# Optimization experiments

Measured on AMD Instinct MI355X. Metric: run time of the kernel, lower is better.

## Reference

```python
import jax, jax.numpy as jnp
import numpy as np

N, E, U, EF, STEPS = 5000, 40000, 64, 16, 4


def setup_inputs() -> dict:
    key = jax.random.key(0)
    ks = jax.random.split(key, 7)
    node_features = jax.random.normal(ks[0], (N, U), dtype=jnp.float32)
    edge_features = jax.random.normal(ks[1], (E, EF), dtype=jnp.float32)
    pair_indices = jax.random.randint(ks[2], (E, 2), 0, N, dtype=jnp.int32)
    # EdgeNetwork params: kernel (efc, nfc*nfc), bias (nfc*nfc,)
    edge_kernel = jax.random.normal(ks[3], (EF, U * U), dtype=jnp.float32) * 0.05
    edge_bias = jnp.zeros((U * U,), dtype=jnp.float32)
    # Keras GRUCell (reset_after=True): kernel (in, 3u), recurrent (u, 3u), bias (2, 3u)
    gru_kernel = jax.random.normal(ks[4], (U, 3 * U), dtype=jnp.float32) * 0.05
    gru_recurrent_kernel = jax.random.normal(ks[5], (U, 3 * U), dtype=jnp.float32) * 0.05
    gru_bias = jnp.zeros((2, 3 * U), dtype=jnp.float32)
    return {
        "node_features": node_features,
        "edge_features": edge_features,
        "pair_indices": pair_indices,
        "edge_kernel": edge_kernel,
        "edge_bias": edge_bias,
        "gru_kernel": gru_kernel,
        "gru_recurrent_kernel": gru_recurrent_kernel,
        "gru_bias": gru_bias,
    }


def _gru_cell(x, h, kernel, rkernel, bias):
    # Keras GRUCell math with reset_after=True
    u = h.shape[-1]
    mx = x @ kernel + bias[0]          # [N, 3u]
    mh = h @ rkernel + bias[1]         # [N, 3u]
    xz, xr, xh = mx[:, :u], mx[:, u:2 * u], mx[:, 2 * u:]
    iz, ir, ih = mh[:, :u], mh[:, u:2 * u], mh[:, 2 * u:]
    z = jax.nn.sigmoid(xz + iz)
    r = jax.nn.sigmoid(xr + ir)
    hh = jnp.tanh(xh + r * ih)
    return z * h + (1.0 - z) * hh


def reference(node_features, edge_features, pair_indices, edge_kernel, edge_bias,
              gru_kernel, gru_recurrent_kernel, gru_bias):
    n = node_features.shape[0]
    u = node_features.shape[1]  # units (pad_length = 0 since nfc == units)
    src = pair_indices[:, 0]
    nbr = pair_indices[:, 1]
    # Edge matrices are loop-invariant: [E, u, u]
    edge_mats = (edge_features @ edge_kernel + edge_bias).reshape(-1, u, u)
    h = node_features
    for _ in range(STEPS):
        nb = h[nbr]                                    # gather [E, u]
        msg = jnp.einsum('eij,ej->ei', edge_mats, nb)  # per-edge matvec
        agg = jax.ops.segment_sum(msg, src, num_segments=n)  # scatter-sum [N, u]
        h = _gru_cell(agg, h, gru_kernel, gru_recurrent_kernel, gru_bias)
    return h
```

## Files before the change

kernel.cpp:

```cpp
#include <hip/hip_runtime.h>
#include <math.h>

#define NN 5000
#define NE 40000
#define UU 64
#define FE 16
#define FEP 17
#define KD (FEP*UU)
#define KH2 (KD/2)
#define LDK (KD+8)
#define NSTEPS 4
#define NT 16
#define NB ((NN+NT-1)/NT)
#define SLOT 40
#define CH 8
#define WBN (UU*KD)
#define GTN (192*64)

typedef _Float16 half8 __attribute__((ext_vector_type(8)));
typedef float f32x4 __attribute__((ext_vector_type(4)));

__device__ __forceinline__ float sigm(float x){ return 1.f/(1.f + __expf(-x)); }
__device__ __forceinline__ int rfl(int x){ return __builtin_amdgcn_readfirstlane(x); }

__global__ void build_k(const float* __restrict__ ek, const float* __restrict__ eb,
                        const float* __restrict__ gk, const float* __restrict__ rk,
                        _Float16* __restrict__ wb, _Float16* __restrict__ gkt,
                        _Float16* __restrict__ rkt, int* __restrict__ deg){
  int tid = blockIdx.x*blockDim.x + threadIdx.x;
  if (tid < NN) deg[tid] = 0;
  if (tid < WBN){
    int i = tid / KD, k = tid - i*KD;
    int f = k >> 6, j = k & 63;
    float v = (f < FE) ? ek[f*4096 + i*64 + j] : eb[i*64 + j];
    wb[tid] = (_Float16)v;
  } else if (tid < WBN + GTN){
    int r = tid - WBN; int n = r >> 6, k = r & 63;
    gkt[r] = (_Float16)gk[k*192 + n];
  } else if (tid < WBN + 2*GTN){
    int r = tid - WBN - GTN; int n = r >> 6, k = r & 63;
    rkt[r] = (_Float16)rk[k*192 + n];
  }
}

__global__ void bucket_k(const int* __restrict__ pair, int* __restrict__ deg,
                         int* __restrict__ eidb){
  int e = blockIdx.x*blockDim.x + threadIdx.x;
  if (e < NE){
    int v = pair[2*e];
    int pos = atomicAdd(&deg[v], 1);
    if (pos < SLOT) eidb[v*SLOT + pos] = e;
  }
}

__global__ __launch_bounds__(512) void prep_k(const int* __restrict__ pair,
                       const float* __restrict__ ef,
                       const int* __restrict__ deg,
                       const int* __restrict__ eidb,
                       int* __restrict__ nbrP, float* __restrict__ efP){
  int w = threadIdx.x >> 6, lane = threadIdx.x & 63;
  int v = blockIdx.x * 8 + w;
  if (v >= NN) return;
  int dg = deg[v]; if (dg > SLOT) dg = SLOT;
  if (lane < dg){
    int e = eidb[v*SLOT + lane];
    int rank = 0;
    for (int j=0; j<dg; ++j){ int ej = eidb[v*SLOT + j]; rank += (ej < e); }
    nbrP[v*SLOT + rank] = pair[2*e + 1];
    const float4* er = (const float4*)(ef + (size_t)e*FE);
    float4* ew = (float4*)(efP + ((size_t)v*SLOT + rank)*FE);
    ew[0] = er[0]; ew[1] = er[1]; ew[2] = er[2]; ew[3] = er[3];
  }
}

__global__ __launch_bounds__(512) void step_k(const float* __restrict__ h_in,
        float* __restrict__ h_out,
        const int* __restrict__ deg, const int* __restrict__ nbrP,
        const float* __restrict__ efP,
        const _Float16* __restrict__ wb, const _Float16* __restrict__ gkt,
        const _Float16* __restrict__ rkt, const float* __restrict__ gb){
  __shared__ _Float16 Gs[NT*LDK];
  __shared__ float    aggP[2][16][68];
  __shared__ _Float16 aggT[16*72];
  __shared__ _Float16 hT[16*72];

  int tid = threadIdx.x;
  int w = tid >> 6, lane = tid & 63;
  int r16 = lane & 15, kh = lane >> 4;
  int vb = blockIdx.x * NT;

  for (int i=tid; i<NT*64; i+=512){
    int lv = i >> 6, j = i & 63; int v = vb + lv;
    hT[lv*72 + j] = (_Float16)((v < NN) ? h_in[(size_t)v*64 + j] : 0.f);
  }

  {
    int v0 = vb + w*2, v1 = v0 + 1;
    int d0 = (v0 < NN) ? deg[v0] : 0; if (d0 > SLOT) d0 = SLOT; d0 = rfl(d0);
    int d1 = (v1 < NN) ? deg[v1] : 0; if (d1 > SLOT) d1 = SLOT; d1 = rfl(d1);
    int nbr0 = (lane < d0) ? nbrP[(size_t)v0*SLOT + lane] : 0;
    int nbr1 = (lane < d1) ? nbrP[(size_t)v1*SLOT + lane] : 0;
    const float* e0base = efP + (size_t)v0*SLOT*FE;
    const float* e1base = efP + (size_t)v1*SLOT*FE;
    float gA[FEP], gB[FEP];
    #pragma unroll
    for (int f=0;f<FEP;++f){ gA[f] = 0.f; gB[f] = 0.f; }
    int dmax = (d0 > d1) ? d0 : d1;
    for (int c0=0; c0<dmax; c0+=CH){
      float hA[CH], hB[CH];
      #pragma unroll
      for (int q=0;q<CH;++q){ int i=c0+q;
        int nA = __shfl(nbr0, i); int nB = __shfl(nbr1, i);
        hA[q] = (i<d0) ? h_in[(size_t)nA*64 + lane] : 0.f;
        hB[q] = (i<d1) ? h_in[(size_t)nB*64 + lane] : 0.f; }
      #pragma unroll
      for (int q=0;q<CH;++q){ int i=c0+q;
        if (i<d0){
          const float4* er = (const float4*)(e0base + (size_t)i*FE);
          float4 e0 = er[0], e1 = er[1], e2 = er[2], e3 = er[3];
          float hj = hA[q];
          gA[ 0]=fmaf(e0.x,hj,gA[ 0]); gA[ 1]=fmaf(e0.y,hj,gA[ 1]);
          gA[ 2]=fmaf(e0.z,hj,gA[ 2]); gA[ 3]=fmaf(e0.w,hj,gA[ 3]);
          gA[ 4]=fmaf(e1.x,hj,gA[ 4]); gA[ 5]=fmaf(e1.y,hj,gA[ 5]);
          gA[ 6]=fmaf(e1.z,hj,gA[ 6]); gA[ 7]=fmaf(e1.w,hj,gA[ 7]);
          gA[ 8]=fmaf(e2.x,hj,gA[ 8]); gA[ 9]=fmaf(e2.y,hj,gA[ 9]);
          gA[10]=fmaf(e2.z,hj,gA[10]); gA[11]=fmaf(e2.w,hj,gA[11]);
          gA[12]=fmaf(e3.x,hj,gA[12]); gA[13]=fmaf(e3.y,hj,gA[13]);
          gA[14]=fmaf(e3.z,hj,gA[14]); gA[15]=fmaf(e3.w,hj,gA[15]);
          gA[16] += hj;
        }
        if (i<d1){
          const float4* er = (const float4*)(e1base + (size_t)i*FE);
          float4 e0 = er[0], e1 = er[1], e2 = er[2], e3 = er[3];
          float hj = hB[q];
          gB[ 0]=fmaf(e0.x,hj,gB[ 0]); gB[ 1]=fmaf(e0.y,hj,gB[ 1]);
          gB[ 2]=fmaf(e0.z,hj,gB[ 2]); gB[ 3]=fmaf(e0.w,hj,gB[ 3]);
          gB[ 4]=fmaf(e1.x,hj,gB[ 4]); gB[ 5]=fmaf(e1.y,hj,gB[ 5]);
          gB[ 6]=fmaf(e1.z,hj,gB[ 6]); gB[ 7]=fmaf(e1.w,hj,gB[ 7]);
          gB[ 8]=fmaf(e2.x,hj,gB[ 8]); gB[ 9]=fmaf(e2.y,hj,gB[ 9]);
          gB[10]=fmaf(e2.z,hj,gB[10]); gB[11]=fmaf(e2.w,hj,gB[11]);
          gB[12]=fmaf(e3.x,hj,gB[12]); gB[13]=fmaf(e3.y,hj,gB[13]);
          gB[14]=fmaf(e3.z,hj,gB[14]); gB[15]=fmaf(e3.w,hj,gB[15]);
          gB[16] += hj;
        } }
    }
    #pragma unroll
    for (int f=0;f<FEP;++f){
      Gs[(w*2  )*LDK + f*64 + lane] = (_Float16)gA[f];
      Gs[(w*2+1)*LDK + f*64 + lane] = (_Float16)gB[f];
    }
  }
  __syncthreads();

  {
    int cg = w & 3, khalf = w >> 2;
    int koff = khalf * KH2;
    f32x4 acc = {0.f,0.f,0.f,0.f};
    const _Float16* ap = Gs + r16*LDK + koff + kh*8;
    const _Float16* bp = wb + (size_t)(cg*16 + r16)*KD + koff + kh*8;
    #pragma unroll 4
    for (int k0=0; k0<KH2; k0+=32){
      half8 a = *(const half8*)(ap + k0);
      half8 b = *(const half8*)(bp + k0);
      acc = __builtin_amdgcn_mfma_f32_16x16x32_f16(a, b, acc, 0, 0, 0);
    }
    #pragma unroll
    for (int r=0;r<4;++r) aggP[khalf][kh*4+r][cg*16 + r16] = acc[r];
  }
  __syncthreads();

  for (int i=tid; i<NT*64; i+=512){
    int rw = i >> 6, cl = i & 63;
    aggT[rw*72 + cl] = (_Float16)(aggP[0][rw][cl] + aggP[1][rw][cl]);
  }
  __syncthreads();

  if (w < 4){
    int uw = w*16 + r16;
    const _Float16* az = aggT + r16*72 + kh*8;
    const _Float16* ah = hT   + r16*72 + kh*8;
    f32x4 mxz={0.f,0.f,0.f,0.f}, mxr=mxz, mxh=mxz, mhz=mxz, mhr=mxz, mhh=mxz;
    #pragma unroll
    for (int ks=0; ks<2; ++ks){
      half8 aa = *(const half8*)(az + ks*32);
      half8 hh = *(const half8*)(ah + ks*32);
      half8 bz = *(const half8*)(gkt + (size_t)(      uw)*64 + ks*32 + kh*8);
      half8 br = *(const half8*)(gkt + (size_t)( 64 + uw)*64 + ks*32 + kh*8);
      half8 bh = *(const half8*)(gkt + (size_t)(128 + uw)*64 + ks*32 + kh*8);
      half8 cz = *(const half8*)(rkt + (size_t)(      uw)*64 + ks*32 + kh*8);
      half8 cr = *(const half8*)(rkt + (size_t)( 64 + uw)*64 + ks*32 + kh*8);
      half8 ch = *(const half8*)(rkt + (size_t)(128 + uw)*64 + ks*32 + kh*8);
      mxz = __builtin_amdgcn_mfma_f32_16x16x32_f16(aa, bz, mxz, 0,0,0);
      mxr = __builtin_amdgcn_mfma_f32_16x16x32_f16(aa, br, mxr, 0,0,0);
      mxh = __builtin_amdgcn_mfma_f32_16x16x32_f16(aa, bh, mxh, 0,0,0);
      mhz = __builtin_amdgcn_mfma_f32_16x16x32_f16(hh, cz, mhz, 0,0,0);
      mhr = __builtin_amdgcn_mfma_f32_16x16x32_f16(hh, cr, mhr, 0,0,0);
      mhh = __builtin_amdgcn_mfma_f32_16x16x32_f16(hh, ch, mhh, 0,0,0);
    }
    float b0z = gb[uw],      b0r = gb[64+uw],  b0h = gb[128+uw];
    float b1z = gb[192+uw],  b1r = gb[256+uw], b1h = gb[320+uw];
    #pragma unroll
    for (int r=0;r<4;++r){
      int row = vb + kh*4 + r;
      if (row < NN){
        float z  = sigm(mxz[r] + b0z + mhz[r] + b1z);
        float rr = sigm(mxr[r] + b0r + mhr[r] + b1r);
        float hc = tanhf(mxh[r] + b0h + rr*(mhh[r] + b1h));
        float hold = h_in[(size_t)row*64 + uw];
        h_out[(size_t)row*64 + uw] = z*hold + (1.f - z)*hc;
      }
    }
  }
}

extern "C" void kernel_launch(void* const* d_in, const int* in_sizes, int n_in,
                              void* d_out, int out_size, void* d_ws, size_t ws_size,
                              hipStream_t stream){
  const float* nodef = (const float*)d_in[0];
  const float* edgef = (const float*)d_in[1];
  const int*   pair  = (const int*)  d_in[2];
  const float* ek    = (const float*)d_in[3];
  const float* ebias = (const float*)d_in[4];
  const float* gk    = (const float*)d_in[5];
  const float* rk    = (const float*)d_in[6];
  const float* gb    = (const float*)d_in[7];

  char* ws = (char*)d_ws;
  size_t o = 0;
  auto carve = [&](size_t bytes)->char*{
    char* p = ws + o; o = (o + bytes + 255) & ~255ULL; return p; };
  int*      deg  = (int*)     carve(NN*sizeof(int));
  int*      eidb = (int*)     carve((size_t)NN*SLOT*sizeof(int));
  int*      nbrP = (int*)     carve((size_t)NN*SLOT*sizeof(int));
  float*    efP  = (float*)   carve((size_t)NN*SLOT*FE*sizeof(float));
  _Float16* wb   = (_Float16*)carve((size_t)WBN*sizeof(_Float16));
  _Float16* gkt  = (_Float16*)carve((size_t)GTN*sizeof(_Float16));
  _Float16* rkt  = (_Float16*)carve((size_t)GTN*sizeof(_Float16));
  float*    hA   = (float*)   carve((size_t)NN*UU*sizeof(float));
  float*    hB   = (float*)   carve((size_t)NN*UU*sizeof(float));

  build_k <<<(WBN+2*GTN+255)/256, 256, 0, stream>>>(ek, ebias, gk, rk, wb, gkt, rkt, deg);
  bucket_k<<<(NE+255)/256, 256, 0, stream>>>(pair, deg, eidb);
  prep_k  <<<(NN+7)/8, 512, 0, stream>>>(pair, edgef, deg, eidb, nbrP, efP);

  const float* hin = nodef;
  for (int s=0; s<NSTEPS; ++s){
    float* hout = (s == NSTEPS-1) ? (float*)d_out : ((s & 1) ? hB : hA);
    step_k<<<NB, 512, 0, stream>>>(hin, hout, deg, nbrP, efP,
                                   wb, gkt, rkt, gb);
    hin = hout;
  }
}
```

Measured before the change: 119.1 us.

## Split fused step kernel into separate gather and MFMA/GRU kernels

Splits each message-passing step into a gather kernel (one wave per node, accumulating edge-feature-weighted neighbor sums into a global fp16 G buffer) and a matmul+GRU kernel that reads G directly from global memory instead of shared memory. The intent is to remove the per-wave two-node imbalance (dmax across paired nodes) and raise occupancy for the latency-bound gather. In exchange, each step adds a kernel launch and a round trip of roughly 11 MB through global memory or L2. G is padded to 5008 rows, so the last block's MFMA reads stay in bounds but pick up uninitialized rows.

```diff
diff --git a/kernel.cpp b/kernel.cpp
--- a/kernel.cpp
+++ b/kernel.cpp
@@ -2,16 +2,17 @@
 #include <math.h>
 
 #define NN 5000
+#define NNP 5008
 #define NE 40000
 #define UU 64
 #define FE 16
 #define FEP 17
 #define KD (FEP*UU)
 #define KH2 (KD/2)
-#define LDK (KD+8)
 #define NSTEPS 4
 #define NT 16
-#define NB ((NN+NT-1)/NT)
+#define NBM ((NN+NT-1)/NT)
+#define NBG (NN/8)
 #define SLOT 40
 #define CH 8
 #define WBN (UU*KD)
@@ -73,13 +74,50 @@
   }
 }
 
-__global__ __launch_bounds__(512) void step_k(const float* __restrict__ h_in,
-        float* __restrict__ h_out,
+__global__ __launch_bounds__(512) void gather_k(const float* __restrict__ h_in,
         const int* __restrict__ deg, const int* __restrict__ nbrP,
-        const float* __restrict__ efP,
+        const float* __restrict__ efP, _Float16* __restrict__ G){
+  int w = threadIdx.x >> 6, lane = threadIdx.x & 63;
+  int v = blockIdx.x * 8 + w;
+  if (v >= NN) return;
+  int dg = deg[v]; if (dg > SLOT) dg = SLOT; dg = rfl(dg);
+  int nbr = (lane < dg) ? nbrP[(size_t)v*SLOT + lane] : 0;
+  const float* ebase = efP + (size_t)v*SLOT*FE;
+  float g[FEP];
+  #pragma unroll
+  for (int f=0;f<FEP;++f) g[f] = 0.f;
+  for (int c0=0; c0<dg; c0+=CH){
+    float hj[CH];
+    #pragma unroll
+    for (int q=0;q<CH;++q){ int i=c0+q;
+      int nb = __shfl(nbr, i);
+      hj[q] = (i<dg) ? h_in[(size_t)nb*64 + lane] : 0.f; }
+    #pragma unroll
+    for (int q=0;q<CH;++q){ int i=c0+q;
+      if (i<dg){
+        const float4* er = (const float4*)(ebase + (size_t)i*FE);
+        float4 e0 = er[0], e1 = er[1], e2 = er[2], e3 = er[3];
+        float hj_ = hj[q];
+        g[ 0]=fmaf(e0.x,hj_,g[ 0]); g[ 1]=fmaf(e0.y,hj_,g[ 1]);
+        g[ 2]=fmaf(e0.z,hj_,g[ 2]); g[ 3]=fmaf(e0.w,hj_,g[ 3]);
+        g[ 4]=fmaf(e1.x,hj_,g[ 4]); g[ 5]=fmaf(e1.y,hj_,g[ 5]);
+        g[ 6]=fmaf(e1.z,hj_,g[ 6]); g[ 7]=fmaf(e1.w,hj_,g[ 7]);
+        g[ 8]=fmaf(e2.x,hj_,g[ 8]); g[ 9]=fmaf(e2.y,hj_,g[ 9]);
+        g[10]=fmaf(e2.z,hj_,g[10]); g[11]=fmaf(e2.w,hj_,g[11]);
+        g[12]=fmaf(e3.x,hj_,g[12]); g[13]=fmaf(e3.y,hj_,g[13]);
+        g[14]=fmaf(e3.z,hj_,g[14]); g[15]=fmaf(e3.w,hj_,g[15]);
+        g[16] += hj_;
+      } }
+  }
+  _Float16* grow = G + (size_t)v*KD;
+  #pragma unroll
+  for (int f=0;f<FEP;++f) grow[f*64 + lane] = (_Float16)g[f];
+}
+
+__global__ __launch_bounds__(512) void mm_k(const float* __restrict__ h_in,
+        float* __restrict__ h_out, const _Float16* __restrict__ G,
         const _Float16* __restrict__ wb, const _Float16* __restrict__ gkt,
         const _Float16* __restrict__ rkt, const float* __restrict__ gb){
-  __shared__ _Float16 Gs[NT*LDK];
   __shared__ float    aggP[2][16][68];
   __shared__ _Float16 aggT[16*72];
   __shared__ _Float16 hT[16*72];
@@ -93,70 +131,13 @@
     int lv = i >> 6, j = i & 63; int v = vb + lv;
     hT[lv*72 + j] = (_Float16)((v < NN) ? h_in[(size_t)v*64 + j] : 0.f);
   }
-
-  {
-    int v0 = vb + w*2, v1 = v0 + 1;
-    int d0 = (v0 < NN) ? deg[v0] : 0; if (d0 > SLOT) d0 = SLOT; d0 = rfl(d0);
-    int d1 = (v1 < NN) ? deg[v1] : 0; if (d1 > SLOT) d1 = SLOT; d1 = rfl(d1);
-    int nbr0 = (lane < d0) ? nbrP[(size_t)v0*SLOT + lane] : 0;
-    int nbr1 = (lane < d1) ? nbrP[(size_t)v1*SLOT + lane] : 0;
-    const float* e0base = efP + (size_t)v0*SLOT*FE;
-    const float* e1base = efP + (size_t)v1*SLOT*FE;
-    float gA[FEP], gB[FEP];
-    #pragma unroll
-    for (int f=0;f<FEP;++f){ gA[f] = 0.f; gB[f] = 0.f; }
-    int dmax = (d0 > d1) ? d0 : d1;
-    for (int c0=0; c0<dmax; c0+=CH){
-      float hA[CH], hB[CH];
-      #pragma unroll
-      for (int q=0;q<CH;++q){ int i=c0+q;
-        int nA = __shfl(nbr0, i); int nB = __shfl(nbr1, i);
-        hA[q] = (i<d0) ? h_in[(size_t)nA*64 + lane] : 0.f;
-        hB[q] = (i<d1) ? h_in[(size_t)nB*64 + lane] : 0.f; }
-      #pragma unroll
-      for (int q=0;q<CH;++q){ int i=c0+q;
-        if (i<d0){
-          const float4* er = (const float4*)(e0base + (size_t)i*FE);
-          float4 e0 = er[0], e1 = er[1], e2 = er[2], e3 = er[3];
-          float hj = hA[q];
-          gA[ 0]=fmaf(e0.x,hj,gA[ 0]); gA[ 1]=fmaf(e0.y,hj,gA[ 1]);
-          gA[ 2]=fmaf(e0.z,hj,gA[ 2]); gA[ 3]=fmaf(e0.w,hj,gA[ 3]);
-          gA[ 4]=fmaf(e1.x,hj,gA[ 4]); gA[ 5]=fmaf(e1.y,hj,gA[ 5]);
-          gA[ 6]=fmaf(e1.z,hj,gA[ 6]); gA[ 7]=fmaf(e1.w,hj,gA[ 7]);
-          gA[ 8]=fmaf(e2.x,hj,gA[ 8]); gA[ 9]=fmaf(e2.y,hj,gA[ 9]);
-          gA[10]=fmaf(e2.z,hj,gA[10]); gA[11]=fmaf(e2.w,hj,gA[11]);
-          gA[12]=fmaf(e3.x,hj,gA[12]); gA[13]=fmaf(e3.y,hj,gA[13]);
-          gA[14]=fmaf(e3.z,hj,gA[14]); gA[15]=fmaf(e3.w,hj,gA[15]);
-          gA[16] += hj;
-        }
-        if (i<d1){
-          const float4* er = (const float4*)(e1base + (size_t)i*FE);
-          float4 e0 = er[0], e1 = er[1], e2 = er[2], e3 = er[3];
-          float hj = hB[q];
-          gB[ 0]=fmaf(e0.x,hj,gB[ 0]); gB[ 1]=fmaf(e0.y,hj,gB[ 1]);
-          gB[ 2]=fmaf(e0.z,hj,gB[ 2]); gB[ 3]=fmaf(e0.w,hj,gB[ 3]);
-          gB[ 4]=fmaf(e1.x,hj,gB[ 4]); gB[ 5]=fmaf(e1.y,hj,gB[ 5]);
-          gB[ 6]=fmaf(e1.z,hj,gB[ 6]); gB[ 7]=fmaf(e1.w,hj,gB[ 7]);
-          gB[ 8]=fmaf(e2.x,hj,gB[ 8]); gB[ 9]=fmaf(e2.y,hj,gB[ 9]);
-          gB[10]=fmaf(e2.z,hj,gB[10]); gB[11]=fmaf(e2.w,hj,gB[11]);
-          gB[12]=fmaf(e3.x,hj,gB[12]); gB[13]=fmaf(e3.y,hj,gB[13]);
-          gB[14]=fmaf(e3.z,hj,gB[14]); gB[15]=fmaf(e3.w,hj,gB[15]);
-          gB[16] += hj;
-        } }
-    }
-    #pragma unroll
-    for (int f=0;f<FEP;++f){
-      Gs[(w*2  )*LDK + f*64 + lane] = (_Float16)gA[f];
-      Gs[(w*2+1)*LDK + f*64 + lane] = (_Float16)gB[f];
-    }
-  }
   __syncthreads();
 
   {
     int cg = w & 3, khalf = w >> 2;
     int koff = khalf * KH2;
     f32x4 acc = {0.f,0.f,0.f,0.f};
-    const _Float16* ap = Gs + r16*LDK + koff + kh*8;
+    const _Float16* ap = G  + (size_t)(vb + r16)*KD + koff + kh*8;
     const _Float16* bp = wb + (size_t)(cg*16 + r16)*KD + koff + kh*8;
     #pragma unroll 4
     for (int k0=0; k0<KH2; k0+=32){
@@ -233,6 +214,7 @@
   int*      eidb = (int*)     carve((size_t)NN*SLOT*sizeof(int));
   int*      nbrP = (int*)     carve((size_t)NN*SLOT*sizeof(int));
   float*    efP  = (float*)   carve((size_t)NN*SLOT*FE*sizeof(float));
+  _Float16* G    = (_Float16*)carve((size_t)NNP*KD*sizeof(_Float16));
   _Float16* wb   = (_Float16*)carve((size_t)WBN*sizeof(_Float16));
   _Float16* gkt  = (_Float16*)carve((size_t)GTN*sizeof(_Float16));
   _Float16* rkt  = (_Float16*)carve((size_t)GTN*sizeof(_Float16));
@@ -246,8 +228,8 @@
   const float* hin = nodef;
   for (int s=0; s<NSTEPS; ++s){
     float* hout = (s == NSTEPS-1) ? (float*)d_out : ((s & 1) ? hB : hA);
-    step_k<<<NB, 512, 0, stream>>>(hin, hout, deg, nbrP, efP,
-                                   wb, gkt, rkt, gb);
+    gather_k<<<NBG, 512, 0, stream>>>(hin, deg, nbrP, efP, G);
+    mm_k    <<<NBM, 512, 0, stream>>>(hin, hout, G, wb, gkt, rkt, gb);
     hin = hout;
   }
 }
```

After: 164.4 us. 38.0% more time.
